# Kernel optimization log

Hardware: AMD Instinct MI355X
Metric: run time of the kernel (lower is better)

Reference implementation:

```python
import jax, jax.numpy as jnp
import numpy as np

B, S, D = 4, 2048, 1024
H, DK, DV = 16, 64, 64


def setup_inputs() -> dict:
    key = jax.random.key(0)
    ks = jax.random.split(key, 9)
    std = 1.0 / np.sqrt(D)
    inp = {
        "x": jax.random.normal(ks[0], (B, S, D), jnp.float32),
        "c": jax.random.normal(ks[1], (B, S, D), jnp.float32),
        "Wq_x": jax.random.normal(ks[2], (D, H * DK), jnp.float32) * std,
        "Wk_x": jax.random.normal(ks[3], (D, H * DK), jnp.float32) * std,
        "Wv_x": jax.random.normal(ks[4], (D, H * DV), jnp.float32) * std,
        "Wq_c": jax.random.normal(ks[5], (D, H * DK), jnp.float32) * std,
        "Wk_c": jax.random.normal(ks[6], (D, H * DK), jnp.float32) * std,
        "Wv_c": jax.random.normal(ks[7], (D, H * DV), jnp.float32) * std,
        "W_proj": jax.random.normal(ks[8], (2 * H * DV, D), jnp.float32) * (1.0 / np.sqrt(2 * H * DV)),
        "b_proj": jnp.zeros((D,), jnp.float32),
    }
    return inp


def _heads(t, hd):
    # [B,S,H*hd] -> [B,H,S,hd]
    b, s, _ = t.shape
    return t.reshape(b, s, H, hd).transpose(0, 2, 1, 3)


def reference(x, c, Wq_x, Wk_x, Wv_x, Wq_c, Wk_c, Wv_c, W_proj, b_proj):
    q = jnp.concatenate([_heads(x @ Wq_x, DK), _heads(c @ Wq_c, DK)], axis=-1)  # [B,H,S,2DK]
    k = jnp.concatenate([_heads(x @ Wk_x, DK), _heads(c @ Wk_c, DK)], axis=-1)
    v = jnp.concatenate([_heads(x @ Wv_x, DV), _heads(c @ Wv_c, DV)], axis=-1)  # [B,H,S,2DV]
    # NOTE: original scales by sqrt(k_dim), not sqrt(2*k_dim) (faithful)
    scores = jnp.einsum("bhqd,bhkd->bhqk", q, k) / np.float32(np.sqrt(DK))
    attn = jax.nn.softmax(scores, axis=-1)
    out = jnp.einsum("bhqk,bhkd->bhqd", attn, v)  # [B,H,S,2DV]
    out = out.transpose(0, 2, 1, 3).reshape(x.shape[0], x.shape[1], -1)  # [B,S,H*2DV]
    return out @ W_proj + b_proj
```

## Files before the change

### kernel.cpp

```cpp
#include <hip/hip_runtime.h>
#include <hip/hip_bf16.h>
#include <stdint.h>

#define BB 4
#define SS 2048
#define DD 1024
#define HH 16
#define DHH 128

typedef __bf16 bf16x8 __attribute__((ext_vector_type(8)));
typedef __bf16 bf16x4 __attribute__((ext_vector_type(4)));
typedef float  f32x4  __attribute__((ext_vector_type(4)));

#define SL2E 0.180336880111186f

#define GLOAD_LDS16(gp, lp) \
  __builtin_amdgcn_global_load_lds((const __attribute__((address_space(1))) unsigned int*)(gp), \
                                   (__attribute__((address_space(3))) unsigned int*)(lp), 16, 0, 0)

__global__ void cast2_kernel(const float* __restrict__ x, const float* __restrict__ c,
                             __bf16* __restrict__ out, int n) {
    int i = (blockIdx.x * blockDim.x + threadIdx.x) * 4;
    const float* src = (i < n) ? (x + i) : (c + (i - n));
    f32x4 v = *(const f32x4*)src;
    bf16x4 o;
    o[0] = (__bf16)v[0]; o[1] = (__bf16)v[1]; o[2] = (__bf16)v[2]; o[3] = (__bf16)v[3];
    *(bf16x4*)(out + i) = o;
}

__global__ void transpose_cast_kernel(const float* __restrict__ in, __bf16* __restrict__ out,
                                      int K, int N) {
    __shared__ float tile[32][33];
    int n0 = blockIdx.x * 32, k0 = blockIdx.y * 32;
    int tx = threadIdx.x, ty = threadIdx.y;
    #pragma unroll
    for (int i = 0; i < 32; i += 8)
        tile[ty + i][tx] = in[(size_t)(k0 + ty + i) * N + n0 + tx];
    __syncthreads();
    #pragma unroll
    for (int i = 0; i < 32; i += 8)
        out[(size_t)(n0 + ty + i) * K + k0 + tx] = (__bf16)tile[tx][ty + i];
}

__global__ void transpose6_kernel(const float* s0, const float* s1, const float* s2,
                                  const float* s3, const float* s4, const float* s5,
                                  __bf16* __restrict__ dst) {
    const float* srcs[6] = {s0, s1, s2, s3, s4, s5};
    const float* __restrict__ in = srcs[blockIdx.z];
    __bf16* __restrict__ out = dst + (size_t)blockIdx.z * 1024 * 1024;
    __shared__ float tile[32][33];
    int n0 = blockIdx.x * 32, k0 = blockIdx.y * 32;
    int tx = threadIdx.x, ty = threadIdx.y;
    #pragma unroll
    for (int i = 0; i < 32; i += 8)
        tile[ty + i][tx] = in[(size_t)(k0 + ty + i) * 1024 + n0 + tx];
    __syncthreads();
    #pragma unroll
    for (int i = 0; i < 32; i += 8)
        out[(size_t)(n0 + ty + i) * 1024 + k0 + tx] = (__bf16)tile[tx][ty + i];
}

template <int EPI>
__global__ void gemm128_kernel(const __bf16* __restrict__ A, const __bf16* __restrict__ Bt,
                               int K, void* __restrict__ outp, int qkv_off,
                               const float* __restrict__ bias) {
    __shared__ __bf16 As[128][32];
    __shared__ __bf16 Bs[128][32];
    const int t = threadIdx.x;
    const int wave = t >> 6, lane = t & 63;
    const int l15 = lane & 15, quad = lane >> 4;
    const int wm = (wave & 1) * 64, wn = (wave >> 1) * 64;
    const int m0 = blockIdx.x * 128, n0 = blockIdx.y * 128;
    const int lrow = lane >> 2;
    const int lcol = (lane & 3) * 8;

    f32x4 acc[4][4] = {};

    for (int k0 = 0; k0 < K; k0 += 32) {
        #pragma unroll
        for (int c2 = 0; c2 < 2; ++c2) {
            int rb = (wave * 2 + c2) * 16;
            GLOAD_LDS16(A  + (size_t)(m0 + rb + lrow) * K + k0 + lcol, &As[rb][0]);
            GLOAD_LDS16(Bt + (size_t)(n0 + rb + lrow) * K + k0 + lcol, &Bs[rb][0]);
        }
        __syncthreads();
        bf16x8 af[4], bfv[4];
        #pragma unroll
        for (int i = 0; i < 4; ++i) af[i]  = *(const bf16x8*)&As[wm + i * 16 + l15][quad * 8];
        #pragma unroll
        for (int i = 0; i < 4; ++i) bfv[i] = *(const bf16x8*)&Bs[wn + i * 16 + l15][quad * 8];
        #pragma unroll
        for (int mi = 0; mi < 4; ++mi)
            #pragma unroll
            for (int ni = 0; ni < 4; ++ni)
                acc[mi][ni] = __builtin_amdgcn_mfma_f32_16x16x32_bf16(af[mi], bfv[ni], acc[mi][ni], 0, 0, 0);
        __syncthreads();
    }

    const size_t nQKV = (size_t)BB * HH * SS * DHH;
    #pragma unroll
    for (int mi = 0; mi < 4; ++mi) {
        #pragma unroll
        for (int ni = 0; ni < 4; ++ni) {
            #pragma unroll
            for (int rr = 0; rr < 4; ++rr) {
                int m = m0 + wm + mi * 16 + quad * 4 + rr;
                int n = n0 + wn + ni * 16 + l15;
                if (EPI == 1) {
                    float* o = (float*)outp;
                    o[(size_t)m * 1024 + n] = acc[mi][ni][rr] + bias[n];
                } else if (EPI == 2) {
                    int h = m >> 6, dl = m & 63;
                    int b = n >> 11, s = n & (SS - 1);
                    __bf16* vt = (__bf16*)outp;
                    vt[(((size_t)b * HH + h) * DHH + dl + qkv_off) * SS + s] = (__bf16)acc[mi][ni][rr];
                } else {
                    int b = m >> 11, s = m & (SS - 1);
                    int n1 = n & 1023;
                    int h = n1 >> 6, d = (n1 & 63) + qkv_off;
                    if (n < 1024) {
                        __bf16* q = (__bf16*)outp;
                        q[(((size_t)b * HH + h) * SS + s) * DHH + d] = (__bf16)(acc[mi][ni][rr] * SL2E);
                    } else {
                        int dsw = (((d >> 3) ^ (s & 15)) << 3) | (d & 7);
                        __bf16* kq = (__bf16*)outp + nQKV;
                        kq[(((size_t)b * HH + h) * SS + s) * DHH + dsw] = (__bf16)acc[mi][ni][rr];
                    }
                }
            }
        }
    }
}

#define LDS_VT 16384
__global__ __launch_bounds__(256, 2)
void attn_kernel(const __bf16* __restrict__ Q, const __bf16* __restrict__ Kg,
                 const __bf16* __restrict__ Vg, __bf16* __restrict__ O) {
    __shared__ __align__(16) char smem[32768];

    const int t = threadIdx.x;
    const int wave = t >> 6, lane = t & 63;
    const int l15 = lane & 15, quad = lane >> 4;
    const int bh = blockIdx.y;
    const int b = bh >> 4, h = bh & 15;
    const int mt = blockIdx.x;
    const size_t base  = (size_t)bh * SS * DHH;
    const size_t vbase = (size_t)bh * DHH * SS;

    int kaddr[4];
    #pragma unroll
    for (int kst = 0; kst < 4; ++kst)
        kaddr[kst] = l15 * 256 + (((4 * kst + quad) ^ l15) & 15) * 16;
    int vaddr[2];
    #pragma unroll
    for (int kst = 0; kst < 2; ++kst)
        vaddr[kst] = LDS_VT + l15 * 128 + (((4 * kst + quad) ^ (l15 & 7)) & 7) * 16;
    int prad[2];
    #pragma unroll
    for (int kst = 0; kst < 2; ++kst)
        prad[kst] = (wave * 32 + l15) * 128 + (((4 * kst + quad) ^ (2 * (l15 >> 2))) & 7) * 16;
    int pwad[4];
    #pragma unroll
    for (int ns = 0; ns < 4; ++ns)
        pwad[ns] = (wave * 32 + quad * 4) * 128 +
                   (((2 * ns + (l15 >> 3)) ^ (2 * quad)) & 7) * 16 + (l15 & 7) * 2;

    const __bf16* kstage = Kg + base + (size_t)wave * 2048 + lane * 8;
    const __bf16* vstage = Vg + vbase + (size_t)(wave * 32 + (lane >> 3)) * SS
                           + ((lane & 7) ^ ((lane >> 3) & 7)) * 8;

    bf16x8 qf[2][4];
    #pragma unroll
    for (int ms = 0; ms < 2; ++ms) {
        int row = mt * 128 + wave * 32 + ms * 16 + l15;
        #pragma unroll
        for (int kst = 0; kst < 4; ++kst)
            qf[ms][kst] = *(const bf16x8*)(Q + base + (size_t)row * DHH + kst * 32 + quad * 8);
    }

    f32x4 oacc[2][8] = {};
    float li_[2][4] = {};

    for (int kt = 0; kt < SS / 64; ++kt) {
        #pragma unroll
        for (int i = 0; i < 4; ++i)
            GLOAD_LDS16(kstage + (size_t)kt * 8192 + i * 512,
                        smem + wave * 4096 + i * 1024);
        #pragma unroll
        for (int i = 0; i < 4; ++i)
            GLOAD_LDS16(vstage + kt * 64 + (size_t)i * 8 * SS,
                        smem + LDS_VT + wave * 4096 + i * 1024);
        __syncthreads();

        f32x4 sc[2][4] = {};
        #pragma unroll
        for (int kst = 0; kst < 4; ++kst) {
            bf16x8 kf[4];
            #pragma unroll
            for (int ns = 0; ns < 4; ++ns)
                kf[ns] = *(const bf16x8*)(smem + kaddr[kst] + 4096 * ns);
            #pragma unroll
            for (int ms = 0; ms < 2; ++ms)
                #pragma unroll
                for (int ns = 0; ns < 4; ++ns)
                    sc[ms][ns] = __builtin_amdgcn_mfma_f32_16x16x32_bf16(qf[ms][kst], kf[ns], sc[ms][ns], 0, 0, 0);
        }

        #pragma unroll
        for (int ms = 0; ms < 2; ++ms)
            #pragma unroll
            for (int ns = 0; ns < 4; ++ns)
                #pragma unroll
                for (int rr = 0; rr < 4; ++rr) {
                    float p = exp2f(sc[ms][ns][rr]);
                    li_[ms][rr] += p;
                    sc[ms][ns][rr] = p;
                }
        __syncthreads();

        #pragma unroll
        for (int ms = 0; ms < 2; ++ms)
            #pragma unroll
            for (int ns = 0; ns < 4; ++ns)
                #pragma unroll
                for (int rr = 0; rr < 4; ++rr)
                    *(__bf16*)(smem + pwad[ns] + 2048 * ms + 128 * rr) = (__bf16)sc[ms][ns][rr];

        #pragma unroll
        for (int kst = 0; kst < 2; ++kst) {
            bf16x8 pa[2];
            #pragma unroll
            for (int ms = 0; ms < 2; ++ms)
                pa[ms] = *(const bf16x8*)(smem + prad[kst] + 2048 * ms);
            #pragma unroll
            for (int ds = 0; ds < 8; ++ds) {
                bf16x8 vf = *(const bf16x8*)(smem + vaddr[kst] + 2048 * ds);
                #pragma unroll
                for (int ms = 0; ms < 2; ++ms)
                    oacc[ms][ds] = __builtin_amdgcn_mfma_f32_16x16x32_bf16(pa[ms], vf, oacc[ms][ds], 0, 0, 0);
            }
        }
        __syncthreads();
    }

    #pragma unroll
    for (int ms = 0; ms < 2; ++ms)
        #pragma unroll
        for (int rr = 0; rr < 4; ++rr) {
            float v = li_[ms][rr];
            v += __shfl_xor(v, 1);
            v += __shfl_xor(v, 2);
            v += __shfl_xor(v, 4);
            v += __shfl_xor(v, 8);
            li_[ms][rr] = 1.f / v;
        }

    #pragma unroll
    for (int ms = 0; ms < 2; ++ms)
        #pragma unroll
        for (int rr = 0; rr < 4; ++rr) {
            int s = mt * 128 + wave * 32 + ms * 16 + quad * 4 + rr;
            size_t ob = ((size_t)b * SS + s) * (HH * DHH) + (size_t)h * DHH;
            #pragma unroll
            for (int ds = 0; ds < 8; ++ds)
                O[ob + ds * 16 + l15] = (__bf16)(oacc[ms][ds][rr] * li_[ms][rr]);
        }
}

extern "C" void kernel_launch(void* const* d_in, const int* in_sizes, int n_in,
                              void* d_out, int out_size, void* d_ws, size_t ws_size,
                              hipStream_t stream) {
    const float* x      = (const float*)d_in[0];
    const float* c      = (const float*)d_in[1];
    const float* Wq_x   = (const float*)d_in[2];
    const float* Wk_x   = (const float*)d_in[3];
    const float* Wv_x   = (const float*)d_in[4];
    const float* Wq_c   = (const float*)d_in[5];
    const float* Wk_c   = (const float*)d_in[6];
    const float* Wv_c   = (const float*)d_in[7];
    const float* W_proj = (const float*)d_in[8];
    const float* b_proj = (const float*)d_in[9];

    const size_t nXC  = (size_t)BB * SS * DD;
    const size_t nW   = (size_t)DD * DD;
    const size_t nWP  = (size_t)(2 * HH * 64) * DD;
    const size_t nQKV = (size_t)BB * HH * SS * DHH;

    __bf16* ws  = (__bf16*)d_ws;
    __bf16* xb  = ws;
    __bf16* cb  = xb + nXC;
    __bf16* wt0 = cb + nXC;
    __bf16* wt2 = wt0 + 2 * nW;
    __bf16* wt3 = wt0 + 3 * nW;
    __bf16* wt5 = wt0 + 5 * nW;
    __bf16* wtp = wt0 + 6 * nW;
    __bf16* Qb  = wtp + nWP;
    __bf16* Kb  = Qb + nQKV;
    __bf16* Vb  = Kb + nQKV;
    __bf16* Ob  = xb;

    cast2_kernel<<<(int)(2 * nXC / 1024), 256, 0, stream>>>(x, c, xb, (int)nXC);

    transpose6_kernel<<<dim3(32, 32, 6), dim3(32, 8), 0, stream>>>(
        Wq_x, Wk_x, Wv_x, Wq_c, Wk_c, Wv_c, wt0);
    transpose_cast_kernel<<<dim3(32, 64), dim3(32, 8), 0, stream>>>(W_proj, wtp, 2048, 1024);

    dim3 gqk(64, 16);
    gemm128_kernel<4><<<gqk, 256, 0, stream>>>(xb, wt0, 1024, Qb, 0,  nullptr);
    gemm128_kernel<4><<<gqk, 256, 0, stream>>>(cb, wt3, 1024, Qb, 64, nullptr);
    dim3 gv(8, 64);
    gemm128_kernel<2><<<gv, 256, 0, stream>>>(wt2, xb, 1024, Vb, 0,  nullptr);
    gemm128_kernel<2><<<gv, 256, 0, stream>>>(wt5, cb, 1024, Vb, 64, nullptr);

    attn_kernel<<<dim3(16, 64), 256, 0, stream>>>(Qb, Kb, Vb, Ob);

    gemm128_kernel<1><<<dim3(64, 8), 256, 0, stream>>>(Ob, wtp, 2048, d_out, 0, b_proj);
}
```

Baseline: 520.2 us.

## Split attention key tile into halves, raise occupancy, and batch projection GEMM launches

The attention inner loop now handles each 64-key tile as two 32-key halves. This shrinks the live score registers and the P staging footprint, and launch bounds are raised to target three blocks per CU. Exp2 switches to the hardware builtin. The paired QK and V projection GEMMs are merged into single launches using blockIdx.z. The extra barrier per half-tile and a possible register-pressure spill at higher occupancy are the main risks.

```diff
diff --git a/kernel.cpp b/kernel.cpp
--- a/kernel.cpp
+++ b/kernel.cpp
@@ -13,6 +13,12 @@
 typedef float  f32x4  __attribute__((ext_vector_type(4)));
 
 #define SL2E 0.180336880111186f
+
+#if __has_builtin(__builtin_amdgcn_exp2f)
+#define EXP2(x) __builtin_amdgcn_exp2f(x)
+#else
+#define EXP2(x) exp2f(x)
+#endif
 
 #define GLOAD_LDS16(gp, lp) \
   __builtin_amdgcn_global_load_lds((const __attribute__((address_space(1))) unsigned int*)(gp), \
@@ -61,9 +67,15 @@
 }
 
 template <int EPI>
-__global__ void gemm128_kernel(const __bf16* __restrict__ A, const __bf16* __restrict__ Bt,
-                               int K, void* __restrict__ outp, int qkv_off,
+__global__ void gemm128_kernel(const __bf16* __restrict__ A0, const __bf16* __restrict__ A1,
+                               const __bf16* __restrict__ B0, const __bf16* __restrict__ B1,
+                               int K, void* __restrict__ outp,
                                const float* __restrict__ bias) {
+    const int z = blockIdx.z;
+    const __bf16* __restrict__ A  = z ? A1 : A0;
+    const __bf16* __restrict__ Bt = z ? B1 : B0;
+    const int qkv_off = z * 64;
+
     __shared__ __bf16 As[128][32];
     __shared__ __bf16 Bs[128][32];
     const int t = threadIdx.x;
@@ -133,7 +145,7 @@
 }
 
 #define LDS_VT 16384
-__global__ __launch_bounds__(256, 2)
+__global__ __launch_bounds__(256, 3)
 void attn_kernel(const __bf16* __restrict__ Q, const __bf16* __restrict__ Kg,
                  const __bf16* __restrict__ Vg, __bf16* __restrict__ O) {
     __shared__ __align__(16) char smem[32768];
@@ -153,17 +165,14 @@
         kaddr[kst] = l15 * 256 + (((4 * kst + quad) ^ l15) & 15) * 16;
     int vaddr[2];
     #pragma unroll
-    for (int kst = 0; kst < 2; ++kst)
-        vaddr[kst] = LDS_VT + l15 * 128 + (((4 * kst + quad) ^ (l15 & 7)) & 7) * 16;
-    int prad[2];
-    #pragma unroll
-    for (int kst = 0; kst < 2; ++kst)
-        prad[kst] = (wave * 32 + l15) * 128 + (((4 * kst + quad) ^ (2 * (l15 >> 2))) & 7) * 16;
-    int pwad[4];
-    #pragma unroll
-    for (int ns = 0; ns < 4; ++ns)
-        pwad[ns] = (wave * 32 + quad * 4) * 128 +
-                   (((2 * ns + (l15 >> 3)) ^ (2 * quad)) & 7) * 16 + (l15 & 7) * 2;
+    for (int hf = 0; hf < 2; ++hf)
+        vaddr[hf] = LDS_VT + l15 * 128 + (((4 * hf + quad) ^ (l15 & 7)) & 7) * 16;
+    int pw[2];
+    #pragma unroll
+    for (int nl = 0; nl < 2; ++nl)
+        pw[nl] = (wave * 32 + quad * 4) * 64 +
+                 (((2 * nl + (l15 >> 3)) ^ quad) & 3) * 16 + (l15 & 7) * 2;
+    const int par = (wave * 32 + l15) * 64 + ((quad ^ (l15 >> 2)) & 3) * 16;
 
     const __bf16* kstage = Kg + base + (size_t)wave * 2048 + lane * 8;
     const __bf16* vstage = Vg + vbase + (size_t)(wave * 32 + (lane >> 3)) * SS
@@ -192,52 +201,46 @@
                         smem + LDS_VT + wave * 4096 + i * 1024);
         __syncthreads();
 
-        f32x4 sc[2][4] = {};
-        #pragma unroll
-        for (int kst = 0; kst < 4; ++kst) {
-            bf16x8 kf[4];
-            #pragma unroll
-            for (int ns = 0; ns < 4; ++ns)
-                kf[ns] = *(const bf16x8*)(smem + kaddr[kst] + 4096 * ns);
+        #pragma unroll
+        for (int hf = 0; hf < 2; ++hf) {
+            f32x4 sx[2][2] = {};
+            #pragma unroll
+            for (int kst = 0; kst < 4; ++kst) {
+                bf16x8 kf0 = *(const bf16x8*)(smem + kaddr[kst] + 8192 * hf);
+                bf16x8 kf1 = *(const bf16x8*)(smem + kaddr[kst] + 8192 * hf + 4096);
+                sx[0][0] = __builtin_amdgcn_mfma_f32_16x16x32_bf16(qf[0][kst], kf0, sx[0][0], 0, 0, 0);
+                sx[1][0] = __builtin_amdgcn_mfma_f32_16x16x32_bf16(qf[1][kst], kf0, sx[1][0], 0, 0, 0);
+                sx[0][1] = __builtin_amdgcn_mfma_f32_16x16x32_bf16(qf[0][kst], kf1, sx[0][1], 0, 0, 0);
+                sx[1][1] = __builtin_amdgcn_mfma_f32_16x16x32_bf16(qf[1][kst], kf1, sx[1][1], 0, 0, 0);
+            }
             #pragma unroll
             for (int ms = 0; ms < 2; ++ms)
                 #pragma unroll
-                for (int ns = 0; ns < 4; ++ns)
-                    sc[ms][ns] = __builtin_amdgcn_mfma_f32_16x16x32_bf16(qf[ms][kst], kf[ns], sc[ms][ns], 0, 0, 0);
-        }
-
-        #pragma unroll
-        for (int ms = 0; ms < 2; ++ms)
-            #pragma unroll
-            for (int ns = 0; ns < 4; ++ns)
+                for (int nl = 0; nl < 2; ++nl)
+                    #pragma unroll
+                    for (int rr = 0; rr < 4; ++rr) {
+                        float p = EXP2(sx[ms][nl][rr]);
+                        li_[ms][rr] += p;
+                        sx[ms][nl][rr] = p;
+                    }
+            __syncthreads();
+
+            #pragma unroll
+            for (int ms = 0; ms < 2; ++ms)
                 #pragma unroll
-                for (int rr = 0; rr < 4; ++rr) {
-                    float p = exp2f(sc[ms][ns][rr]);
-                    li_[ms][rr] += p;
-                    sc[ms][ns][rr] = p;
-                }
-        __syncthreads();
-
-        #pragma unroll
-        for (int ms = 0; ms < 2; ++ms)
-            #pragma unroll
-            for (int ns = 0; ns < 4; ++ns)
-                #pragma unroll
-                for (int rr = 0; rr < 4; ++rr)
-                    *(__bf16*)(smem + pwad[ns] + 2048 * ms + 128 * rr) = (__bf16)sc[ms][ns][rr];
-
-        #pragma unroll
-        for (int kst = 0; kst < 2; ++kst) {
-            bf16x8 pa[2];
-            #pragma unroll
-            for (int ms = 0; ms < 2; ++ms)
-                pa[ms] = *(const bf16x8*)(smem + prad[kst] + 2048 * ms);
+                for (int nl = 0; nl < 2; ++nl)
+                    #pragma unroll
+                    for (int rr = 0; rr < 4; ++rr)
+                        *(__bf16*)(smem + pw[nl] + 8192 * hf + 1024 * ms + 64 * rr)
+                            = (__bf16)sx[ms][nl][rr];
+
+            bf16x8 pa0 = *(const bf16x8*)(smem + par + 8192 * hf);
+            bf16x8 pa1 = *(const bf16x8*)(smem + par + 8192 * hf + 1024);
             #pragma unroll
             for (int ds = 0; ds < 8; ++ds) {
-                bf16x8 vf = *(const bf16x8*)(smem + vaddr[kst] + 2048 * ds);
-                #pragma unroll
-                for (int ms = 0; ms < 2; ++ms)
-                    oacc[ms][ds] = __builtin_amdgcn_mfma_f32_16x16x32_bf16(pa[ms], vf, oacc[ms][ds], 0, 0, 0);
+                bf16x8 vf = *(const bf16x8*)(smem + vaddr[hf] + 2048 * ds);
+                oacc[0][ds] = __builtin_amdgcn_mfma_f32_16x16x32_bf16(pa0, vf, oacc[0][ds], 0, 0, 0);
+                oacc[1][ds] = __builtin_amdgcn_mfma_f32_16x16x32_bf16(pa1, vf, oacc[1][ds], 0, 0, 0);
             }
         }
         __syncthreads();
@@ -305,14 +308,10 @@
         Wq_x, Wk_x, Wv_x, Wq_c, Wk_c, Wv_c, wt0);
     transpose_cast_kernel<<<dim3(32, 64), dim3(32, 8), 0, stream>>>(W_proj, wtp, 2048, 1024);
 
-    dim3 gqk(64, 16);
-    gemm128_kernel<4><<<gqk, 256, 0, stream>>>(xb, wt0, 1024, Qb, 0,  nullptr);
-    gemm128_kernel<4><<<gqk, 256, 0, stream>>>(cb, wt3, 1024, Qb, 64, nullptr);
-    dim3 gv(8, 64);
-    gemm128_kernel<2><<<gv, 256, 0, stream>>>(wt2, xb, 1024, Vb, 0,  nullptr);
-    gemm128_kernel<2><<<gv, 256, 0, stream>>>(wt5, cb, 1024, Vb, 64, nullptr);
+    gemm128_kernel<4><<<dim3(64, 16, 2), 256, 0, stream>>>(xb, cb, wt0, wt3, 1024, Qb, nullptr);
+    gemm128_kernel<2><<<dim3(8, 64, 2), 256, 0, stream>>>(wt2, wt5, xb, cb, 1024, Vb, nullptr);
 
     attn_kernel<<<dim3(16, 64), 256, 0, stream>>>(Qb, Kb, Vb, Ob);
 
-    gemm128_kernel<1><<<dim3(64, 8), 256, 0, stream>>>(Ob, wtp, 2048, d_out, 0, b_proj);
-}
+    gemm128_kernel<1><<<dim3(64, 8, 1), 256, 0, stream>>>(Ob, nullptr, wtp, nullptr, 2048, d_out, b_proj);
+}
```

Result: faster. 488.4 us (-6.1%).
